# Optimization experiments

Measured on AMD Instinct MI355X. Metric: run time of the kernel, lower is better.

The kernel has to match this reference:

```python
import jax
import jax.numpy as jnp
import numpy as np
from jax import lax

DIM = 48
HIDDEN = int(DIM * 2.66)  # 127, matches torch int(dim*ffn_expansion_factor)
EPS_LN = 1e-5
EPS_NORM = 1e-12


def conv2d(x, w, groups=1):
    # x: NCHW, w: OIHW, stride 1, SAME padding (all kernels here are 1x1 or 3x3 pad=1)
    return lax.conv_general_dilated(
        x, w, window_strides=(1, 1), padding='SAME',
        feature_group_count=groups,
        dimension_numbers=('NCHW', 'OIHW', 'NCHW'))


def layernorm_cbias(x, w, b):
    # Restormer WithBias_LayerNorm: normalize over channel dim (biased var)
    mu = jnp.mean(x, axis=1, keepdims=True)
    var = jnp.mean(jnp.square(x - mu), axis=1, keepdims=True)
    xn = (x - mu) * lax.rsqrt(var + EPS_LN)
    return xn * w[None, :, None, None] + b[None, :, None, None]


def l2norm_last(x):
    # torch F.normalize(dim=-1, eps=1e-12)
    n = jnp.sqrt(jnp.sum(jnp.square(x), axis=-1, keepdims=True))
    return x / jnp.maximum(n, EPS_NORM)


def setup_inputs() -> dict:
    key = jax.random.key(0)
    ks = jax.random.split(key, 16)
    s = 0.05
    B, H, W = 2, 512, 512
    return {
        'x': jax.random.normal(ks[0], (B, 3, H, W), dtype=jnp.float32),
        # OverlapPatchEmbed: Conv2d(3, 48, 3, pad=1, bias=False)
        'pe_w': jax.random.normal(ks[1], (DIM, 3, 3, 3), dtype=jnp.float32) * s,
        # norm1 (WithBias)
        'n1_w': jnp.ones((DIM,), dtype=jnp.float32),
        'n1_b': jnp.zeros((DIM,), dtype=jnp.float32),
        # MDTA attention, num_heads=1
        'temp': jnp.ones((1, 1, 1), dtype=jnp.float32),
        'qkv_w': jax.random.normal(ks[2], (DIM * 3, DIM, 1, 1), dtype=jnp.float32) * s,
        'qkv_dw_w': jax.random.normal(ks[3], (DIM * 3, 1, 3, 3), dtype=jnp.float32) * s,
        'po_w': jax.random.normal(ks[4], (DIM, DIM, 1, 1), dtype=jnp.float32) * s,
        # norm2
        'n2_w': jnp.ones((DIM,), dtype=jnp.float32),
        'n2_b': jnp.zeros((DIM,), dtype=jnp.float32),
        # GDFN
        'pi_w': jax.random.normal(ks[5], (HIDDEN * 2, DIM, 1, 1), dtype=jnp.float32) * s,
        'ffn_dw_w': jax.random.normal(ks[6], (HIDDEN * 2, 1, 3, 3), dtype=jnp.float32) * s,
        'fo_w': jax.random.normal(ks[7], (DIM, HIDDEN, 1, 1), dtype=jnp.float32) * s,
    }


def reference(x, pe_w, n1_w, n1_b, temp, qkv_w, qkv_dw_w, po_w, n2_w, n2_b, pi_w, ffn_dw_w, fo_w):
    # Patch embed
    patch = conv2d(x, pe_w)  # [B, 48, H, W]
    B, C, H, W = patch.shape

    # ---- MDTA channel attention on norm1(patch) ----
    y = layernorm_cbias(patch, n1_w, n1_b)
    qkv = conv2d(conv2d(y, qkv_w), qkv_dw_w, groups=3 * C)  # [B, 3C, H, W]
    q, k, v = jnp.split(qkv, 3, axis=1)
    # heads=1: rearrange to [B, C, H*W]
    q = l2norm_last(q.reshape(B, C, H * W))
    k = l2norm_last(k.reshape(B, C, H * W))
    v = v.reshape(B, C, H * W)
    attn = jax.nn.softmax(jnp.einsum('bcn,bdn->bcd', q, k) * temp[0, 0, 0], axis=-1)  # [B, C, C]
    out = jnp.einsum('bcd,bdn->bcn', attn, v).reshape(B, C, H, W)
    attn_out = conv2d(out, po_w)
    first = patch + attn_out

    # ---- GDFN on norm2(first) ----
    y2 = layernorm_cbias(first, n2_w, n2_b)
    h = conv2d(conv2d(y2, pi_w), ffn_dw_w, groups=2 * HIDDEN)  # [B, 254, H, W]
    x1, x2 = jnp.split(h, 2, axis=1)
    ffn = conv2d(jax.nn.gelu(x1, approximate=False) * x2, fo_w)
    return first + ffn  # second_residual [B, 48, H, W]
```

## Files before the change

kernel.cpp:

```cpp
#include <hip/hip_runtime.h>
#include <hip/hip_bf16.h>
#include <math.h>

#define HW 512
#define NPIX (HW*HW)

typedef __hip_bfloat16 bf16;
typedef __attribute__((ext_vector_type(8))) unsigned short u16x8;
typedef __attribute__((ext_vector_type(8))) short s16x8;
typedef __attribute__((ext_vector_type(4))) float f32x4;

__device__ __forceinline__ float b2f(bf16 v) { return __bfloat162float(v); }
__device__ __forceinline__ bf16 f2b(float v) { return __float2bfloat16(v); }

union fu { float f; unsigned int u; };
union bu { bf16 b; unsigned short u; };

__device__ __forceinline__ float us2f(unsigned short u) {
    fu c; c.u = ((unsigned int)u) << 16; return c.f;
}

__device__ __forceinline__ void ld_bf8(const bf16* p, float* f) {
    u16x8 u = *(const u16x8*)p;
#pragma unroll
    for (int j = 0; j < 8; j++) { fu c; c.u = ((unsigned int)u[j]) << 16; f[j] = c.f; }
}

__device__ __forceinline__ void st_bf8(bf16* p, const float* f) {
    u16x8 u;
#pragma unroll
    for (int j = 0; j < 8; j++) { bu c; c.b = f2b(f[j]); u[j] = c.u; }
    *(u16x8*)p = u;
}

__global__ __launch_bounds__(256) void k_prep(const float* __restrict__ qkvw,
                                              const float* __restrict__ piw,
                                              const float* __restrict__ fow,
                                              bf16* __restrict__ WQ,
                                              bf16* __restrict__ WP,
                                              bf16* __restrict__ WF,
                                              float* __restrict__ Z0,
                                              float* __restrict__ Z1)
{
    int idx = blockIdx.x*256 + threadIdx.x;
    if (idx < 9216) {
        int oc = idx >> 6, k = idx & 63;
        WQ[idx] = f2b(k < 48 ? qkvw[oc*48 + k] : 0.f);
    } else if (idx < 25600) {
        int j = idx - 9216; int oc = j >> 6, k = j & 63;
        WP[j] = f2b((oc < 254 && k < 48) ? piw[oc*48 + k] : 0.f);
    } else if (idx < 31744) {
        int j = idx - 25600; int oc = j >> 7, k = j & 127;
        WF[j] = f2b(k < 127 ? fow[oc*127 + k] : 0.f);
    } else if (idx < 36544) {
        int j = idx - 31744;
        if (j < 2400) Z0[j] = 0.f; else Z1[j-2400] = 0.f;
    }
}

__global__ __launch_bounds__(256) void k_pe(const float* __restrict__ x,
                                            const float* __restrict__ w,
                                            bf16* __restrict__ out)
{
    __shared__ float ws[48*27];
    for (int i = threadIdx.x; i < 48*27; i += 256) ws[i] = w[i];
    __syncthreads();
    int lane = threadIdx.x & 63, wv = threadIdx.x >> 6;
    int row = blockIdx.x*4 + wv;
    int col = lane*8;
    float a[3][3][8];
    float lf[3][3], rt[3][3];
#pragma unroll
    for (int c = 0; c < 3; c++)
#pragma unroll
        for (int r = 0; r < 3; r++) {
            int rr = row + r - 1;
            if (rr >= 0 && rr < HW) {
                const float* p = x + (size_t)c*NPIX + rr*HW + col;
                float4 u0 = *(const float4*)p, u1 = *(const float4*)(p+4);
                a[c][r][0]=u0.x; a[c][r][1]=u0.y; a[c][r][2]=u0.z; a[c][r][3]=u0.w;
                a[c][r][4]=u1.x; a[c][r][5]=u1.y; a[c][r][6]=u1.z; a[c][r][7]=u1.w;
            } else {
#pragma unroll
                for (int j = 0; j < 8; j++) a[c][r][j] = 0.f;
            }
            float l = __shfl_up(a[c][r][7], 1);  lf[c][r] = (lane==0)  ? 0.f : l;
            float rv= __shfl_down(a[c][r][0],1); rt[c][r] = (lane==63) ? 0.f : rv;
        }
    for (int oc = 0; oc < 48; oc++) {
        float acc[8];
#pragma unroll
        for (int j = 0; j < 8; j++) acc[j] = 0.f;
#pragma unroll
        for (int c = 0; c < 3; c++)
#pragma unroll
            for (int r = 0; r < 3; r++) {
                float w0 = ws[oc*27 + c*9 + r*3 + 0];
                float w1 = ws[oc*27 + c*9 + r*3 + 1];
                float w2 = ws[oc*27 + c*9 + r*3 + 2];
#pragma unroll
                for (int j = 0; j < 8; j++) {
                    float xm = (j==0) ? lf[c][r] : a[c][r][j-1];
                    float x0 = a[c][r][j];
                    float xp = (j==7) ? rt[c][r] : a[c][r][j+1];
                    acc[j] += w0*xm + w1*x0 + w2*xp;
                }
            }
        st_bf8(out + (size_t)oc*NPIX + row*HW + col, acc);
    }
}

#define YPAD 48
#define CHS 408
__global__ __launch_bounds__(256) void k_ln_dw(const bf16* __restrict__ patch,
                                               const float* __restrict__ lnw,
                                               const float* __restrict__ lnb,
                                               const s16x8* __restrict__ wq,
                                               const float* __restrict__ dww,
                                               bf16* __restrict__ outq)
{
    __shared__ unsigned short y_lds[400*YPAD];
    __shared__ unsigned short a_lds[48*CHS];
    int t = threadIdx.x;
    int c0 = blockIdx.x*32, r0 = blockIdx.y*8;

    for (int p = t; p < 400; p += 256) {
        int hr = p/40, hc = p - hr*40;
        int gr = r0 - 1 + hr, gc = c0 - 1 + hc;
        bool ok = (hc < 34) && (gr >= 0) && (gr < HW) && (gc >= 0) && (gc < HW);
        if (ok) {
            int gpx = gr*HW + gc;
            float y[48];
            float mu = 0.f;
#pragma unroll
            for (int i = 0; i < 48; i++) { y[i] = b2f(patch[(size_t)i*NPIX + gpx]); mu += y[i]; }
            mu *= (1.f/48.f);
            float var = 0.f;
#pragma unroll
            for (int i = 0; i < 48; i++) { float d = y[i]-mu; var += d*d; }
            float s = rsqrtf(var*(1.f/48.f) + 1e-5f);
#pragma unroll
            for (int i = 0; i < 48; i++) y[i] = (y[i]-mu)*s*lnw[i] + lnb[i];
#pragma unroll
            for (int kb = 0; kb < 6; kb++) {
                union { u16x8 v; unsigned short us[8]; } pk;
#pragma unroll
                for (int j = 0; j < 8; j++) { bu b; b.b = f2b(y[kb*8+j]); pk.us[j] = b.u; }
                *(u16x8*)&y_lds[p*YPAD + kb*8] = pk.v;
            }
        } else {
            u16x8 z = {0,0,0,0,0,0,0,0};
#pragma unroll
            for (int kb = 0; kb < 6; kb++) *(u16x8*)&y_lds[p*YPAD + kb*8] = z;
        }
    }
    __syncthreads();

    int lane = t & 63, wv = t >> 6;
    int q = lane >> 4, n = lane & 15;
    int ch2 = lane >> 5;
    int idx5 = lane & 31;
    int orow = idx5 >> 2;
    int cg   = idx5 & 3;

#pragma unroll 1
    for (int cc = 0; cc < 3; cc++) {
        s16x8 w0[3], w1[3];
#pragma unroll
        for (int mi = 0; mi < 3; mi++) {
            int oc = (cc*3 + mi)*16 + n;
            w0[mi] = wq[oc*8 + q];
            w1[mi] = wq[oc*8 + 4 + q];
        }
#pragma unroll 1
        for (int nt = wv; nt < 25; nt += 4) {
            int p16 = nt*16;
            s16x8 ya = *(const s16x8*)&y_lds[(p16 + n)*YPAD + q*8];
            s16x8 yb = {0,0,0,0,0,0,0,0};
            if (q < 2) yb = *(const s16x8*)&y_lds[(p16 + n)*YPAD + 32 + q*8];
#pragma unroll
            for (int mi = 0; mi < 3; mi++) {
                f32x4 acc = {0.f, 0.f, 0.f, 0.f};
                acc = __builtin_amdgcn_mfma_f32_16x16x32_bf16(ya, w0[mi], acc, 0, 0, 0);
                acc = __builtin_amdgcn_mfma_f32_16x16x32_bf16(yb, w1[mi], acc, 0, 0, 0);
                union { unsigned short us[4]; ushort4 v; } pk;
#pragma unroll
                for (int r = 0; r < 4; r++) { bu bb; bb.b = f2b(acc[r]); pk.us[r] = bb.u; }
                *(ushort4*)&a_lds[(mi*16 + n)*CHS + p16 + q*4] = pk.v;
            }
        }
        __syncthreads();

#pragma unroll 1
        for (int i = 0; i < 6; i++) {
            int chl = i*8 + wv*2 + ch2;
            int ch  = cc*48 + chl;
            float wk[9];
#pragma unroll
            for (int k = 0; k < 9; k++) wk[k] = dww[ch*9 + k];
            const unsigned short* ap = &a_lds[chl*CHS];
            float win[3][10];
#pragma unroll
            for (int kr = 0; kr < 3; kr++) {
                u16x8 A = *(const u16x8*)&ap[(orow + kr)*40 + cg*8];
                unsigned int B = *(const unsigned int*)&ap[(orow + kr)*40 + cg*8 + 8];
#pragma unroll
                for (int j = 0; j < 8; j++) win[kr][j] = us2f(A[j]);
                win[kr][8] = us2f((unsigned short)(B & 0xffffu));
                win[kr][9] = us2f((unsigned short)(B >> 16));
            }
            u16x8 pk;
#pragma unroll
            for (int j = 0; j < 8; j++) {
                float sm = 0.f;
#pragma unroll
                for (int kr = 0; kr < 3; kr++)
                    sm += wk[kr*3+0]*win[kr][j] + wk[kr*3+1]*win[kr][j+1] + wk[kr*3+2]*win[kr][j+2];
                bu b; b.b = f2b(sm); pk[j] = b.u;
            }
            *(u16x8*)&outq[(size_t)ch*NPIX + (r0 + orow)*HW + c0 + cg*8] = pk;
        }
        __syncthreads();
    }
}

template<int OC_PAD, int OC_REAL, int MT_PER_WAVE>
__global__ __launch_bounds__(256) void k_ln_mm_mfma(const bf16* __restrict__ in,
                                                    const float* __restrict__ lnw,
                                                    const float* __restrict__ lnb,
                                                    const s16x8* __restrict__ wpad,
                                                    bf16* __restrict__ out)
{
    constexpr int NMT = OC_PAD/16;
    __shared__ s16x8 y_lds[256*8];
    __shared__ unsigned short stage[OC_PAD][72];
    int t = threadIdx.x;
    int base = blockIdx.x*256;
    int px = base + t;
    float y[48];
    float mu = 0.f;
#pragma unroll
    for (int i = 0; i < 48; i++) { y[i] = b2f(in[(size_t)i*NPIX + px]); mu += y[i]; }
    mu *= (1.f/48.f);
    float var = 0.f;
#pragma unroll
    for (int i = 0; i < 48; i++) { float d = y[i]-mu; var += d*d; }
    float s = rsqrtf(var*(1.f/48.f) + 1e-5f);
#pragma unroll
    for (int i = 0; i < 48; i++) y[i] = (y[i]-mu)*s*lnw[i] + lnb[i];
#pragma unroll
    for (int kb = 0; kb < 8; kb++) {
        union { s16x8 v; unsigned short us[8]; } pk;
#pragma unroll
        for (int j = 0; j < 8; j++) {
            int c = kb*8 + j;
            bu b; b.b = f2b(c < 48 ? y[c] : 0.f);
            pk.us[j] = (c < 48) ? b.u : (unsigned short)0;
        }
        y_lds[t*8 + (kb ^ (t & 7))] = pk.v;
    }
    __syncthreads();

    int lane = t & 63, wv = t >> 6;
    int q = lane >> 4, n = lane & 15;
    s16x8 a[MT_PER_WAVE][2];
#pragma unroll
    for (int mi = 0; mi < MT_PER_WAVE; mi++) {
        int mt = wv + 4*mi;
        if (mt < NMT) {
            int oc = mt*16 + n;
            a[mi][0] = wpad[oc*8 + q];
            a[mi][1] = wpad[oc*8 + 4 + q];
        }
    }
#pragma unroll 1
    for (int g = 0; g < 4; g++) {
#pragma unroll
        for (int sub = 0; sub < 4; sub++) {
            int nt = g*4 + sub;
            int npx = nt*16 + n;
            s16x8 b0 = y_lds[npx*8 + (q ^ (npx & 7))];
            s16x8 b1 = y_lds[npx*8 + ((4 + q) ^ (npx & 7))];
#pragma unroll
            for (int mi = 0; mi < MT_PER_WAVE; mi++) {
                int mt = wv + 4*mi;
                if (mt >= NMT) continue;
                f32x4 acc = {0.f, 0.f, 0.f, 0.f};
                acc = __builtin_amdgcn_mfma_f32_16x16x32_bf16(b0, a[mi][0], acc, 0, 0, 0);
                acc = __builtin_amdgcn_mfma_f32_16x16x32_bf16(b1, a[mi][1], acc, 0, 0, 0);
                int oc = mt*16 + n;
                union { unsigned short us[4]; ushort4 v; } pk;
#pragma unroll
                for (int r = 0; r < 4; r++) { bu bb; bb.b = f2b(acc[r]); pk.us[r] = bb.u; }
                *(ushort4*)&stage[oc][sub*16 + q*4] = pk.v;
            }
        }
        __syncthreads();
        if (t < OC_REAL) {
            const u16x8* sp = (const u16x8*)stage[t];
            u16x8 c0 = sp[0], c1 = sp[1], c2 = sp[2], c3 = sp[3];
            u16x8 c4 = sp[4], c5 = sp[5], c6 = sp[6], c7 = sp[7];
            u16x8* op = (u16x8*)(out + (size_t)t*NPIX + base + g*64);
            op[0] = c0; op[1] = c1; op[2] = c2; op[3] = c3;
            op[4] = c4; op[5] = c5; op[6] = c6; op[7] = c7;
        }
        __syncthreads();
    }
}

__global__ __launch_bounds__(512) void k_qkt(const bf16* __restrict__ qm,
                                             const bf16* __restrict__ km,
                                             float* __restrict__ S,
                                             float* __restrict__ sumsq)
{
    __shared__ float Sp[8][48][52];
    __shared__ float ssp[8][96];
    int t = threadIdx.x;
    int lane = t & 63, wv = t >> 6;
    int qg = lane >> 4, n = lane & 15;
    size_t px0 = (size_t)(blockIdx.x*8 + wv) * 64 + qg*8;

    f32x4 acc[3][3];
#pragma unroll
    for (int i = 0; i < 3; i++)
#pragma unroll
        for (int j = 0; j < 3; j++) acc[i][j] = (f32x4){0.f, 0.f, 0.f, 0.f};
    float sq[3] = {0.f, 0.f, 0.f}, sk[3] = {0.f, 0.f, 0.f};

#pragma unroll
    for (int s = 0; s < 2; s++) {
        size_t p = px0 + s*32;
        s16x8 qa[3], ka[3];
#pragma unroll
        for (int i = 0; i < 3; i++) {
            qa[i] = *(const s16x8*)&qm[(size_t)(16*i + n)*NPIX + p];
            ka[i] = *(const s16x8*)&km[(size_t)(16*i + n)*NPIX + p];
        }
#pragma unroll
        for (int i = 0; i < 3; i++)
#pragma unroll
            for (int j = 0; j < 3; j++)
                acc[i][j] = __builtin_amdgcn_mfma_f32_16x16x32_bf16(qa[i], ka[j], acc[i][j], 0, 0, 0);
#pragma unroll
        for (int i = 0; i < 3; i++) {
            union { s16x8 v; unsigned short us[8]; } uq, uk;
            uq.v = qa[i]; uk.v = ka[i];
#pragma unroll
            for (int j = 0; j < 8; j++) {
                fu cq; cq.u = ((unsigned int)uq.us[j]) << 16; sq[i] += cq.f*cq.f;
                fu ck; ck.u = ((unsigned int)uk.us[j]) << 16; sk[i] += ck.f*ck.f;
            }
        }
    }

#pragma unroll
    for (int i = 0; i < 3; i++)
#pragma unroll
        for (int j = 0; j < 3; j++)
#pragma unroll
            for (int r = 0; r < 4; r++)
                Sp[wv][16*i + qg*4 + r][16*j + n] = acc[i][j][r];
#pragma unroll
    for (int i = 0; i < 3; i++) {
        float a = sq[i], b = sk[i];
        a += __shfl_down(a, 32); a += __shfl_down(a, 16);
        b += __shfl_down(b, 32); b += __shfl_down(b, 16);
        if (lane < 16) { ssp[wv][16*i + lane] = a; ssp[wv][48 + 16*i + lane] = b; }
    }
    __syncthreads();

    for (int idx = t; idx < 2304; idx += 512) {
        int r = idx / 48, c = idx - r*48;
        float v = 0.f;
#pragma unroll
        for (int w = 0; w < 8; w++) v += Sp[w][r][c];
        atomicAdd(&S[idx], v);
    }
    if (t < 96) {
        float v = 0.f;
#pragma unroll
        for (int w = 0; w < 8; w++) v += ssp[w][t];
        atomicAdd(&sumsq[t], v);
    }
}

__global__ __launch_bounds__(256) void k_attn_final(const float* __restrict__ S,
                                                    const float* __restrict__ sumsq,
                                                    const float* __restrict__ po_w,
                                                    const float* __restrict__ temp,
                                                    float* __restrict__ M)
{
    __shared__ float attn[48][48];
    __shared__ float nrm[96];
    int t = threadIdx.x;
    if (t < 96) nrm[t] = fmaxf(sqrtf(sumsq[t]), 1e-12f);
    __syncthreads();
    float tmp = temp[0];
    if (t < 48) {
        float row[48];
        float mx = -1e30f;
#pragma unroll
        for (int d = 0; d < 48; d++) {
            float l = S[t*48+d] / (nrm[t]*nrm[48+d]) * tmp;
            row[d] = l; mx = fmaxf(mx, l);
        }
        float sum = 0.f;
#pragma unroll
        for (int d = 0; d < 48; d++) { float e = expf(row[d]-mx); sum += e; row[d] = e; }
        float inv = 1.f/sum;
#pragma unroll
        for (int d = 0; d < 48; d++) attn[t][d] = row[d]*inv;
    }
    __syncthreads();
    for (int idx = t; idx < 2304; idx += 256) {
        int cp = idx/48, d = idx%48;
        float acc = 0.f;
#pragma unroll
        for (int c = 0; c < 48; c++) acc += po_w[cp*48+c] * attn[c][d];
        M[idx] = acc;
    }
}

__global__ __launch_bounds__(256) void k_attnv(const bf16* __restrict__ v,
                                               const float* __restrict__ M,
                                               bf16* __restrict__ patch)
{
    __shared__ float Ms[48*48];
    for (int i = threadIdx.x; i < 2304; i += 256) Ms[i] = M[i];
    __syncthreads();
    int p = (blockIdx.x*256 + threadIdx.x)*2;
    float v0[48], v1[48];
#pragma unroll
    for (int i = 0; i < 48; i++) {
        unsigned int word = *(const unsigned int*)&v[(size_t)i*NPIX + p];
        fu c0, c1; c0.u = word << 16; c1.u = word & 0xffff0000u;
        v0[i] = c0.f; v1[i] = c1.f;
    }
    for (int oc = 0; oc < 48; oc++) {
        const float4* wr = (const float4*)&Ms[oc*48];
        float a0 = 0.f, a1 = 0.f;
#pragma unroll
        for (int i = 0; i < 12; i++) {
            float4 w4 = wr[i];
            a0 += w4.x*v0[4*i] + w4.y*v0[4*i+1] + w4.z*v0[4*i+2] + w4.w*v0[4*i+3];
            a1 += w4.x*v1[4*i] + w4.y*v1[4*i+1] + w4.z*v1[4*i+2] + w4.w*v1[4*i+3];
        }
        unsigned int* pp = (unsigned int*)&patch[(size_t)oc*NPIX + p];
        unsigned int old = *pp;
        fu f0, f1; f0.u = old << 16; f1.u = old & 0xffff0000u;
        bu b0, b1; b0.b = f2b(f0.f + a0); b1.b = f2b(f1.f + a1);
        *pp = (unsigned int)b0.u | ((unsigned int)b1.u << 16);
    }
}

__global__ __launch_bounds__(256) void k_dw_glu(const bf16* __restrict__ h1,
                                                const float* __restrict__ w,
                                                bf16* __restrict__ g)
{
    int ch = blockIdx.y;
    int lane = threadIdx.x & 63, wv = threadIdx.x >> 6;
    int row0 = blockIdx.x*32 + wv*8;
    int col = lane*8;
    float w1[9], w2[9];
#pragma unroll
    for (int i = 0; i < 9; i++) { w1[i] = w[ch*9+i]; w2[i] = w[(ch+127)*9+i]; }
    const bf16* i1 = h1 + (size_t)ch*NPIX;
    const bf16* i2 = h1 + (size_t)(ch+127)*NPIX;
    bf16* op = g + (size_t)ch*NPIX;
    float aa[4][8], bb[4][8];
    float lfa[4], rta[4], lfb[4], rtb[4];

    auto loadraw = [&](int s, int rr) {
        if (rr >= 0 && rr < HW) {
            ld_bf8(i1 + rr*HW + col, aa[s]);
            ld_bf8(i2 + rr*HW + col, bb[s]);
        } else {
#pragma unroll
            for (int j = 0; j < 8; j++) { aa[s][j] = 0.f; bb[s][j] = 0.f; }
        }
    };
    auto doshfl = [&](int s) {
        float l1 = __shfl_up(aa[s][7],1);   lfa[s] = (lane==0)  ? 0.f : l1;
        float r1 = __shfl_down(aa[s][0],1); rta[s] = (lane==63) ? 0.f : r1;
        float l2 = __shfl_up(bb[s][7],1);   lfb[s] = (lane==0)  ? 0.f : l2;
        float r2 = __shfl_down(bb[s][0],1); rtb[s] = (lane==63) ? 0.f : r2;
    };

    loadraw(0, row0-1);
    loadraw(1, row0);
    loadraw(2, row0+1);
    doshfl(0);
    doshfl(1);
#pragma unroll
    for (int r = 0; r < 8; r++) {
        if (r < 7) loadraw((r+3)&3, row0 + r + 2);
        doshfl((r+2)&3);
        const int s0 = r&3, s1 = (r+1)&3, s2 = (r+2)&3;
        float o[8];
#pragma unroll
        for (int j = 0; j < 8; j++) {
            float sum1 = 0.f, sum2 = 0.f;
#pragma unroll
            for (int kr = 0; kr < 3; kr++) {
                const int ss = (kr==0) ? s0 : (kr==1) ? s1 : s2;
                float xm = (j==0) ? lfa[ss] : aa[ss][j-1];
                float x0 = aa[ss][j];
                float xp = (j==7) ? rta[ss] : aa[ss][j+1];
                sum1 += w1[kr*3+0]*xm + w1[kr*3+1]*x0 + w1[kr*3+2]*xp;
                float ym = (j==0) ? lfb[ss] : bb[ss][j-1];
                float y0 = bb[ss][j];
                float yp = (j==7) ? rtb[ss] : bb[ss][j+1];
                sum2 += w2[kr*3+0]*ym + w2[kr*3+1]*y0 + w2[kr*3+2]*yp;
            }
            float ge = 0.5f*sum1*(1.f + erff(sum1*0.70710678118654752f));
            o[j] = ge*sum2;
        }
        st_bf8(op + (row0 + r)*HW + col, o);
    }
}

__global__ __launch_bounds__(256) void k_fo_mfma(const bf16* __restrict__ g,
                                                 const s16x8* __restrict__ wfo,
                                                 const bf16* __restrict__ first,
                                                 float* __restrict__ out)
{
    __shared__ s16x8 glds[256*16];
    int t = threadIdx.x;
    int base = blockIdx.x*256;
    int px = base + t;
#pragma unroll
    for (int kb = 0; kb < 16; kb++) {
        union { s16x8 v; unsigned short us[8]; } pk;
#pragma unroll
        for (int j = 0; j < 8; j++) {
            int c = kb*8 + j;
            if (c < 127) { bu b; b.b = g[(size_t)c*NPIX + px]; pk.us[j] = b.u; }
            else pk.us[j] = 0;
        }
        glds[t*16 + (kb ^ (t & 15))] = pk.v;
    }
    __syncthreads();
    int lane = t & 63, wv = t >> 6;
    int q = lane >> 4, n = lane & 15;
    s16x8 a[3][4];
#pragma unroll
    for (int mt = 0; mt < 3; mt++) {
        int oc = mt*16 + n;
#pragma unroll
        for (int kc = 0; kc < 4; kc++)
            a[mt][kc] = wfo[oc*16 + kc*4 + q];
    }
#pragma unroll 1
    for (int ni = 0; ni < 4; ni++) {
        int nt = wv*4 + ni;
        int npx = nt*16 + n;
        s16x8 b[4];
#pragma unroll
        for (int kc = 0; kc < 4; kc++)
            b[kc] = glds[npx*16 + ((kc*4 + q) ^ (npx & 15))];
        size_t px4 = (size_t)base + nt*16 + q*4;
#pragma unroll
        for (int mt = 0; mt < 3; mt++) {
            f32x4 acc = {0.f, 0.f, 0.f, 0.f};
#pragma unroll
            for (int kc = 0; kc < 4; kc++)
                acc = __builtin_amdgcn_mfma_f32_16x16x32_bf16(b[kc], a[mt][kc], acc, 0, 0, 0);
            int oc = mt*16 + n;
            ushort4 fr = *(const ushort4*)&first[(size_t)oc*NPIX + px4];
            float4 o;
            o.x = us2f(fr.x) + acc[0];
            o.y = us2f(fr.y) + acc[1];
            o.z = us2f(fr.z) + acc[2];
            o.w = us2f(fr.w) + acc[3];
            *(float4*)&out[(size_t)oc*NPIX + px4] = o;
        }
    }
}

extern "C" void kernel_launch(void* const* d_in, const int* in_sizes, int n_in,
                              void* d_out, int out_size, void* d_ws, size_t ws_size,
                              hipStream_t stream)
{
    const float* x     = (const float*)d_in[0];
    const float* pe_w  = (const float*)d_in[1];
    const float* n1w   = (const float*)d_in[2];
    const float* n1b   = (const float*)d_in[3];
    const float* temp  = (const float*)d_in[4];
    const float* qkvw  = (const float*)d_in[5];
    const float* qkvdw = (const float*)d_in[6];
    const float* pow_  = (const float*)d_in[7];
    const float* n2w   = (const float*)d_in[8];
    const float* n2b   = (const float*)d_in[9];
    const float* piw   = (const float*)d_in[10];
    const float* ffndw = (const float*)d_in[11];
    const float* fow   = (const float*)d_in[12];
    float* out = (float*)d_out;

    bf16*  Pb = (bf16*)d_ws;
    bf16*  A  = Pb + (size_t)48*NPIX;
    bf16*  Bq = A + (size_t)144*NPIX;
    bf16*  H1 = A;
    bf16*  G  = A + (size_t)254*NPIX;
    bf16*  WQ = A + (size_t)381*NPIX;
    bf16*  WP = WQ + 144*64;
    bf16*  WF = WP + 256*64;
    float* SM0 = (float*)(A + (size_t)384*NPIX);
    float* SM1 = SM0 + 4704;

    dim3 blk(256);
    int nb1 = NPIX/256;
    int nb2 = NPIX/512;
    int nr  = HW/4;
    int nrw = HW/32;

    k_prep<<<dim3(143), blk, 0, stream>>>(qkvw, piw, fow, WQ, WP, WF, SM0, SM1);

    for (int b = 0; b < 2; b++) {
        const float* xb   = x   + (size_t)b*3*NPIX;
        float*       outb = out + (size_t)b*48*NPIX;
        float* SMb   = b ? SM1 : SM0;
        float* sumsq = SMb;
        float* S     = SMb + 96;
        float* M     = SMb + 2400;

        k_pe<<<dim3(nr), blk, 0, stream>>>(xb, pe_w, Pb);
        k_ln_dw<<<dim3(HW/32, HW/8), blk, 0, stream>>>(Pb, n1w, n1b, (const s16x8*)WQ, qkvdw, Bq);
        k_qkt<<<dim3(NPIX/512), dim3(512), 0, stream>>>(Bq, Bq + (size_t)48*NPIX, S, sumsq);
        k_attn_final<<<dim3(1), blk, 0, stream>>>(S, sumsq, pow_, temp, M);
        k_attnv<<<dim3(nb2), blk, 0, stream>>>(Bq + (size_t)96*NPIX, M, Pb);
        k_ln_mm_mfma<256,254,4><<<dim3(nb1), blk, 0, stream>>>(Pb, n2w, n2b, (const s16x8*)WP, H1);
        k_dw_glu<<<dim3(nrw, 127), blk, 0, stream>>>(H1, ffndw, G);
        k_fo_mfma<<<dim3(nb1), blk, 0, stream>>>(G, (const s16x8*)WF, Pb, outb);
    }
}
```

Baseline: 728.8 us.

## Halve LDS staging in LN-matmul and FFN-out kernels to raise occupancy

```diff
diff --git a/kernel.cpp b/kernel.cpp
--- a/kernel.cpp
+++ b/kernel.cpp
@@ -233,7 +233,7 @@
 {
     constexpr int NMT = OC_PAD/16;
     __shared__ s16x8 y_lds[256*8];
-    __shared__ unsigned short stage[OC_PAD][72];
+    __shared__ unsigned short stage[OC_PAD/2][72];
     int t = threadIdx.x;
     int base = blockIdx.x*256;
     int px = base + t;
@@ -275,36 +275,42 @@
     }
 #pragma unroll 1
     for (int g = 0; g < 4; g++) {
-#pragma unroll
-        for (int sub = 0; sub < 4; sub++) {
-            int nt = g*4 + sub;
-            int npx = nt*16 + n;
-            s16x8 b0 = y_lds[npx*8 + (q ^ (npx & 7))];
-            s16x8 b1 = y_lds[npx*8 + ((4 + q) ^ (npx & 7))];
-#pragma unroll
-            for (int mi = 0; mi < MT_PER_WAVE; mi++) {
-                int mt = wv + 4*mi;
-                if (mt >= NMT) continue;
-                f32x4 acc = {0.f, 0.f, 0.f, 0.f};
-                acc = __builtin_amdgcn_mfma_f32_16x16x32_bf16(b0, a[mi][0], acc, 0, 0, 0);
-                acc = __builtin_amdgcn_mfma_f32_16x16x32_bf16(b1, a[mi][1], acc, 0, 0, 0);
-                int oc = mt*16 + n;
-                union { unsigned short us[4]; ushort4 v; } pk;
-#pragma unroll
-                for (int r = 0; r < 4; r++) { bu bb; bb.b = f2b(acc[r]); pk.us[r] = bb.u; }
-                *(ushort4*)&stage[oc][sub*16 + q*4] = pk.v;
-            }
-        }
-        __syncthreads();
-        if (t < OC_REAL) {
-            const u16x8* sp = (const u16x8*)stage[t];
-            u16x8 c0 = sp[0], c1 = sp[1], c2 = sp[2], c3 = sp[3];
-            u16x8 c4 = sp[4], c5 = sp[5], c6 = sp[6], c7 = sp[7];
-            u16x8* op = (u16x8*)(out + (size_t)t*NPIX + base + g*64);
-            op[0] = c0; op[1] = c1; op[2] = c2; op[3] = c3;
-            op[4] = c4; op[5] = c5; op[6] = c6; op[7] = c7;
-        }
-        __syncthreads();
+#pragma unroll 1
+        for (int half = 0; half < 2; half++) {
+#pragma unroll
+            for (int sub = 0; sub < 4; sub++) {
+                int nt = g*4 + sub;
+                int npx = nt*16 + n;
+                s16x8 b0 = y_lds[npx*8 + (q ^ (npx & 7))];
+                s16x8 b1 = y_lds[npx*8 + ((4 + q) ^ (npx & 7))];
+#pragma unroll
+                for (int mh = 0; mh < 2; mh++) {
+                    int mi = half*2 + mh;
+                    int mt = wv + 4*mi;
+                    f32x4 acc = {0.f, 0.f, 0.f, 0.f};
+                    acc = __builtin_amdgcn_mfma_f32_16x16x32_bf16(b0, a[mi][0], acc, 0, 0, 0);
+                    acc = __builtin_amdgcn_mfma_f32_16x16x32_bf16(b1, a[mi][1], acc, 0, 0, 0);
+                    int srow = (mt - half*8)*16 + n;
+                    union { unsigned short us[4]; ushort4 v; } pk;
+#pragma unroll
+                    for (int r = 0; r < 4; r++) { bu bb; bb.b = f2b(acc[r]); pk.us[r] = bb.u; }
+                    *(ushort4*)&stage[srow][sub*16 + q*4] = pk.v;
+                }
+            }
+            __syncthreads();
+            if (t < 128) {
+                int oc = half*128 + t;
+                if (oc < OC_REAL) {
+                    const u16x8* sp = (const u16x8*)stage[t];
+                    u16x8 c0 = sp[0], c1 = sp[1], c2 = sp[2], c3 = sp[3];
+                    u16x8 c4 = sp[4], c5 = sp[5], c6 = sp[6], c7 = sp[7];
+                    u16x8* op = (u16x8*)(out + (size_t)oc*NPIX + base + g*64);
+                    op[0] = c0; op[1] = c1; op[2] = c2; op[3] = c3;
+                    op[4] = c4; op[5] = c5; op[6] = c6; op[7] = c7;
+                }
+            }
+            __syncthreads();
+        }
     }
 }
 
@@ -524,24 +530,14 @@
                                                  const bf16* __restrict__ first,
                                                  float* __restrict__ out)
 {
-    __shared__ s16x8 glds[256*16];
+    __shared__ s16x8 glds[128*16];
     int t = threadIdx.x;
     int base = blockIdx.x*256;
-    int px = base + t;
-#pragma unroll
-    for (int kb = 0; kb < 16; kb++) {
-        union { s16x8 v; unsigned short us[8]; } pk;
-#pragma unroll
-        for (int j = 0; j < 8; j++) {
-            int c = kb*8 + j;
-            if (c < 127) { bu b; b.b = g[(size_t)c*NPIX + px]; pk.us[j] = b.u; }
-            else pk.us[j] = 0;
-        }
-        glds[t*16 + (kb ^ (t & 15))] = pk.v;
-    }
-    __syncthreads();
     int lane = t & 63, wv = t >> 6;
     int q = lane >> 4, n = lane & 15;
+    int hpx = t & 127;
+    int kb0 = (t >> 7) * 8;
+
     s16x8 a[3][4];
 #pragma unroll
     for (int mt = 0; mt < 3; mt++) {
@@ -550,30 +546,50 @@
         for (int kc = 0; kc < 4; kc++)
             a[mt][kc] = wfo[oc*16 + kc*4 + q];
     }
+
 #pragma unroll 1
-    for (int ni = 0; ni < 4; ni++) {
-        int nt = wv*4 + ni;
-        int npx = nt*16 + n;
-        s16x8 b[4];
-#pragma unroll
-        for (int kc = 0; kc < 4; kc++)
-            b[kc] = glds[npx*16 + ((kc*4 + q) ^ (npx & 15))];
-        size_t px4 = (size_t)base + nt*16 + q*4;
-#pragma unroll
-        for (int mt = 0; mt < 3; mt++) {
-            f32x4 acc = {0.f, 0.f, 0.f, 0.f};
+    for (int h = 0; h < 2; h++) {
+        int px = base + h*128 + hpx;
+#pragma unroll
+        for (int jj = 0; jj < 8; jj++) {
+            int kb = kb0 + jj;
+            union { s16x8 v; unsigned short us[8]; } pk;
+#pragma unroll
+            for (int j = 0; j < 8; j++) {
+                int c = kb*8 + j;
+                if (c < 127) { bu b; b.b = g[(size_t)c*NPIX + px]; pk.us[j] = b.u; }
+                else pk.us[j] = 0;
+            }
+            glds[hpx*16 + (kb ^ (hpx & 15))] = pk.v;
+        }
+        __syncthreads();
+
+#pragma unroll 1
+        for (int ni = 0; ni < 2; ni++) {
+            int nt = wv*2 + ni;
+            int npx = nt*16 + n;
+            s16x8 b[4];
 #pragma unroll
             for (int kc = 0; kc < 4; kc++)
-                acc = __builtin_amdgcn_mfma_f32_16x16x32_bf16(b[kc], a[mt][kc], acc, 0, 0, 0);
-            int oc = mt*16 + n;
-            ushort4 fr = *(const ushort4*)&first[(size_t)oc*NPIX + px4];
-            float4 o;
-            o.x = us2f(fr.x) + acc[0];
-            o.y = us2f(fr.y) + acc[1];
-            o.z = us2f(fr.z) + acc[2];
-            o.w = us2f(fr.w) + acc[3];
-            *(float4*)&out[(size_t)oc*NPIX + px4] = o;
-        }
+                b[kc] = glds[npx*16 + ((kc*4 + q) ^ (npx & 15))];
+            size_t px4 = (size_t)base + h*128 + nt*16 + q*4;
+#pragma unroll
+            for (int mt = 0; mt < 3; mt++) {
+                f32x4 acc = {0.f, 0.f, 0.f, 0.f};
+#pragma unroll
+                for (int kc = 0; kc < 4; kc++)
+                    acc = __builtin_amdgcn_mfma_f32_16x16x32_bf16(b[kc], a[mt][kc], acc, 0, 0, 0);
+                int oc = mt*16 + n;
+                ushort4 fr = *(const ushort4*)&first[(size_t)oc*NPIX + px4];
+                float4 o;
+                o.x = us2f(fr.x) + acc[0];
+                o.y = us2f(fr.y) + acc[1];
+                o.z = us2f(fr.z) + acc[2];
+                o.w = us2f(fr.w) + acc[3];
+                *(float4*)&out[(size_t)oc*NPIX + px4] = o;
+            }
+        }
+        __syncthreads();
     }
 }
 
```

After: 1.591 ms. 118% more time.
